# Kernel optimization log

Measured on AMD Instinct MI355X. Metric: run time of the kernel, lower is better.

## Reference

```python
import jax, jax.numpy as jnp
import numpy as np

N, E, NG = 10000, 160000, 64
HID, HEADS = 256, 4
NEG_SLOPE = 0.2


def setup_inputs() -> dict:
    key = jax.random.key(0)
    ks = jax.random.split(key, 20)
    s = 0.1
    inp = {
        "atom_features": jax.random.normal(ks[0], (N, 23), jnp.float32),
        "edge_index": jax.random.randint(ks[1], (2, E), 0, N),
        "batch": jnp.sort(jax.random.randint(ks[2], (N,), 0, NG)),
        "W1": jax.random.normal(ks[3], (23, HEADS * HID), jnp.float32) * s,
        "as1": jax.random.normal(ks[4], (HEADS, HID), jnp.float32) * s,
        "ad1": jax.random.normal(ks[5], (HEADS, HID), jnp.float32) * s,
        "b1": jnp.zeros((HEADS * HID,), jnp.float32),
        "W2": jax.random.normal(ks[6], (HEADS * HID, HEADS * HID), jnp.float32) * s,
        "as2": jax.random.normal(ks[7], (HEADS, HID), jnp.float32) * s,
        "ad2": jax.random.normal(ks[8], (HEADS, HID), jnp.float32) * s,
        "b2": jnp.zeros((HEADS * HID,), jnp.float32),
        "W3": jax.random.normal(ks[9], (HEADS * HID, HID), jnp.float32) * s,
        "as3": jax.random.normal(ks[10], (1, HID), jnp.float32) * s,
        "ad3": jax.random.normal(ks[11], (1, HID), jnp.float32) * s,
        "b3": jnp.zeros((HID,), jnp.float32),
        # MLP head
        "fc1_w": jax.random.normal(ks[12], (HID, HID // 2), jnp.float32) * s,
        "fc1_b": jnp.zeros((HID // 2,), jnp.float32),
        "fc2_w": jax.random.normal(ks[13], (HID // 2, 1), jnp.float32) * s,
        "fc2_b": jnp.zeros((1,), jnp.float32),
    }
    return inp


def gat_layer(x, W, att_src, att_dst, bias, src, dst, heads, ch):
    n = x.shape[0]
    h = (x @ W).reshape(n, heads, ch)                      # [N,H,C]
    a_s = jnp.sum(h * att_src, axis=-1)                    # [N,H]
    a_d = jnp.sum(h * att_dst, axis=-1)                    # [N,H]
    logits = jax.nn.leaky_relu(a_s[src] + a_d[dst], NEG_SLOPE)  # [E',H]
    m = jax.ops.segment_max(logits, dst, num_segments=n)
    m = jnp.where(jnp.isfinite(m), m, 0.0)
    e = jnp.exp(logits - m[dst])
    denom = jax.ops.segment_sum(e, dst, num_segments=n)
    alpha = e / (denom[dst] + 1e-16)                       # segment softmax over incoming edges
    out = jax.ops.segment_sum(alpha[:, :, None] * h[src], dst, num_segments=n)
    return out.reshape(n, heads * ch) + bias


def reference(atom_features, edge_index, batch,
              W1, as1, ad1, b1, W2, as2, ad2, b2, W3, as3, ad3, b3,
              fc1_w, fc1_b, fc2_w, fc2_b):
    n = atom_features.shape[0]
    loops = jnp.arange(n)
    src = jnp.concatenate([edge_index[0], loops])   # PyG GATConv adds self-loops
    dst = jnp.concatenate([edge_index[1], loops])

    x = jax.nn.elu(gat_layer(atom_features, W1, as1, ad1, b1, src, dst, HEADS, HID))
    x = jax.nn.elu(gat_layer(x, W2, as2, ad2, b2, src, dst, HEADS, HID))
    x = jax.nn.elu(gat_layer(x, W3, as3, ad3, b3, src, dst, 1, HID))
    # dropout: eval mode (training=False) -> identity

    # global mean pool over molecules
    sums = jax.ops.segment_sum(x, batch, num_segments=NG)
    counts = jax.ops.segment_sum(jnp.ones((n,), x.dtype), batch, num_segments=NG)
    features = sums / jnp.maximum(counts, 1.0)[:, None]    # [NG, HID]

    hmid = jax.nn.relu(features @ fc1_w + fc1_b)
    validity = hmid @ fc2_w + fc2_b                        # [NG, 1]
    return validity, features
```

## Files before the change

kernel.cpp:

```cpp
#include <hip/hip_runtime.h>
#include <hip/hip_bf16.h>
#include <math.h>

typedef unsigned short ushortT;
typedef __attribute__((ext_vector_type(8))) short short8;
typedef __attribute__((ext_vector_type(4))) float f32x4;

constexpr int NN   = 10000;
constexpr int MP   = 10112;
constexpr int EE   = 160000;
constexpr int ETOT = EE + NN;
constexpr int NG   = 64;
constexpr int HID  = 256;
constexpr int HEADS = 4;

__device__ __forceinline__ ushortT f2bf(float x) {
    __hip_bfloat16 h = __float2bfloat16(x);
    return *reinterpret_cast<ushortT*>(&h);
}
__device__ __forceinline__ float bf2f(ushortT x) {
    unsigned u = ((unsigned)x) << 16;
    return __uint_as_float(u);
}

__device__ __forceinline__ int xcd_swz(int flat, int nwg) {
    int q = nwg >> 3, r = nwg & 7;
    int xcd = flat & 7, j = flat >> 3;
    return (xcd < r ? xcd * (q + 1) : r * (q + 1) + (xcd - r) * q) + j;
}

__global__ __launch_bounds__(256) void setup_kernel(
        const float* __restrict__ W1, const float* __restrict__ as1,
        const float* __restrict__ ad1, float* __restrict__ wsv1,
        const float* __restrict__ W2, const float* __restrict__ as2,
        const float* __restrict__ ad2, float* __restrict__ wsv2,
        const float* __restrict__ W3, const float* __restrict__ as3,
        const float* __restrict__ ad3, float* __restrict__ wsv3,
        ushortT* __restrict__ wt2, ushortT* __restrict__ wt3,
        ushortT* __restrict__ b1p, const int* __restrict__ ei,
        int* __restrict__ cnt) {
    __shared__ float t[32][33];
    const int b = blockIdx.x, tid = threadIdx.x;
    if (b < 1280) {
        const float* W; ushortT* Wt; int N, n0, k0;
        if (b < 1024) { W = W2; Wt = wt2; N = 1024; n0 = (b & 31) * 32; k0 = (b >> 5) * 32; }
        else          { int b2 = b - 1024; W = W3; Wt = wt3; N = 256; n0 = (b2 & 7) * 32; k0 = (b2 >> 3) * 32; }
        const int K = 1024, Kp = 1024;
        int tx = tid & 31, ty = tid >> 5;
        for (int i = ty; i < 32; i += 8) {
            int k = k0 + i, n = n0 + tx;
            t[i][tx] = (k < K && n < N) ? W[(size_t)k * N + n] : 0.f;
        }
        __syncthreads();
        for (int i = ty; i < 32; i += 8) {
            int n = n0 + i, kp = k0 + tx;
            if (n < N && kp < Kp) Wt[(size_t)n * Kp + kp] = f2bf(t[tx][i]);
        }
    } else if (b < 1792) {
        int idx = (b - 1280) * 256 + tid;
        int n = idx >> 7, kp = idx & 127;
        int h = n >> 8, hk = kp >> 5, k = kp & 31;
        float v = (hk == h && k < 23) ? W1[(size_t)k * 1024 + n] : 0.f;
        b1p[idx] = f2bf(v);
    } else if (b < 4398) {
        int gw = (b - 1792) * 4 + (tid >> 6);
        int lane = tid & 63;
        const float *W, *atts, *attd; float* wsv; int heads, idx;
        if (gw < 184)            { W = W1; atts = as1; attd = ad1; wsv = wsv1; heads = 4; idx = gw; }
        else if (gw < 184 + 8192){ W = W2; atts = as2; attd = ad2; wsv = wsv2; heads = 4; idx = gw - 184; }
        else if (gw < 184 + 8192 + 2048) { W = W3; atts = as3; attd = ad3; wsv = wsv3; heads = 1; idx = gw - 184 - 8192; }
        else return;
        const int nout = 2 * heads;
        int k = idx / nout, o = idx - k * nout;
        int h = (o >= heads) ? (o - heads) : o;
        const float* att  = ((o >= heads) ? attd : atts) + h * HID;
        const float* wrow = W + (size_t)k * (heads * HID) + h * HID;
        float4 w4 = *(const float4*)(wrow + lane * 4);
        float4 a4 = *(const float4*)(att + lane * 4);
        float s = w4.x * a4.x + w4.y * a4.y + w4.z * a4.z + w4.w * a4.w;
        #pragma unroll
        for (int off = 1; off < 64; off <<= 1) s += __shfl_xor(s, off);
        if (lane == 0) wsv[(size_t)k * nout + o] = s;
    } else {
        int e = (b - 4398) * 256 + tid;
        if (e >= ETOT) return;
        int dst = (e < EE) ? ei[EE + e] : (e - EE);
        atomicAdd(&cnt[dst], 1);
    }
}

__global__ void scan_kernel(const int* __restrict__ cnt, int* __restrict__ row_ptr,
                            int* __restrict__ cursor) {
    __shared__ int part[256];
    int tid = threadIdx.x;
    const int chunk = (NN + 255) / 256;
    int s0 = tid * chunk;
    int s1 = min(NN, s0 + chunk);
    int sum = 0;
    for (int i = s0; i < s1; ++i) sum += cnt[i];
    part[tid] = sum;
    __syncthreads();
    for (int off = 1; off < 256; off <<= 1) {
        int v = (tid >= off) ? part[tid - off] : 0;
        __syncthreads();
        part[tid] += v;
        __syncthreads();
    }
    int run = (tid == 0) ? 0 : part[tid - 1];
    for (int i = s0; i < s1; ++i) {
        row_ptr[i] = run;
        cursor[i]  = run;
        run += cnt[i];
    }
    if (tid == 255) row_ptr[NN] = part[255];
}

__global__ void fill_dots1_kernel(const int* __restrict__ ei, int* __restrict__ cursor,
                                  int* __restrict__ col_src,
                                  const float* __restrict__ atom,
                                  const float* __restrict__ wsv1,
                                  float* __restrict__ a_s, float* __restrict__ a_d,
                                  int nfill) {
    int b = blockIdx.x;
    if (b < nfill) {
        int e = b * 256 + threadIdx.x;
        if (e >= ETOT) return;
        int src, dst;
        if (e < EE) { src = ei[e]; dst = ei[EE + e]; }
        else        { src = dst = e - EE; }
        int pos = atomicAdd(&cursor[dst], 1);
        col_src[pos] = src;
    } else {
        int n = (b - nfill) * 256 + threadIdx.x;
        if (n >= NN) return;
        float a[8] = {0.f, 0.f, 0.f, 0.f, 0.f, 0.f, 0.f, 0.f};
        #pragma unroll
        for (int k = 0; k < 23; ++k) {
            float x = atom[n * 23 + k];
            #pragma unroll
            for (int o = 0; o < 8; ++o) a[o] += x * wsv1[k * 8 + o];
        }
        #pragma unroll
        for (int h = 0; h < 4; ++h) { a_s[n * 4 + h] = a[h]; a_d[n * 4 + h] = a[4 + h]; }
    }
}

__global__ __launch_bounds__(256) void agg_atom_kernel(const float* __restrict__ atom,
                                                       const float* __restrict__ a_s,
                                                       const float* __restrict__ a_d,
                                                       const int* __restrict__ rowp,
                                                       const int* __restrict__ colv,
                                                       ushortT* __restrict__ Ap) {
    const int wv = threadIdx.x >> 6, lane = threadIdx.x & 63;
    const int i = blockIdx.x * 4 + wv;
    if (i >= NN) return;
    const int half = lane >> 5, c = lane & 31;
    const int start = rowp[i], end = rowp[i + 1];

    __shared__ float wsh[4][64][4];
    __shared__ int   ssh[4][64];

    float acc[4] = {0.f, 0.f, 0.f, 0.f};
    float den4[4] = {0.f, 0.f, 0.f, 0.f};
    for (int cb = start; cb < end; cb += 64) {
        int clen = min(64, end - cb);
        if (lane < clen) {
            int s = colv[cb + lane];
            ssh[wv][lane] = s;
            float4 as4 = *(const float4*)(a_s + (size_t)s * 4);
            float4 ad4 = *(const float4*)(a_d + (size_t)i * 4);
            float l0 = as4.x + ad4.x; l0 = (l0 >= 0.f) ? l0 : 0.2f * l0;
            float l1 = as4.y + ad4.y; l1 = (l1 >= 0.f) ? l1 : 0.2f * l1;
            float l2 = as4.z + ad4.z; l2 = (l2 >= 0.f) ? l2 : 0.2f * l2;
            float l3 = as4.w + ad4.w; l3 = (l3 >= 0.f) ? l3 : 0.2f * l3;
            float w0 = expf(l0), w1 = expf(l1), w2 = expf(l2), w3 = expf(l3);
            *reinterpret_cast<float4*>(&wsh[wv][lane][0]) = make_float4(w0, w1, w2, w3);
            den4[0] += w0; den4[1] += w1; den4[2] += w2; den4[3] += w3;
        }
        __builtin_amdgcn_wave_barrier();
        for (int e = half; e < clen; e += 2) {
            int s = ssh[wv][e];
            float x = (c < 23) ? atom[(size_t)s * 23 + c] : 0.f;
            acc[0] += wsh[wv][e][0] * x;
            acc[1] += wsh[wv][e][1] * x;
            acc[2] += wsh[wv][e][2] * x;
            acc[3] += wsh[wv][e][3] * x;
        }
        __builtin_amdgcn_wave_barrier();
    }
    #pragma unroll
    for (int h = 0; h < 4; ++h) acc[h] += __shfl_xor(acc[h], 32);
    #pragma unroll
    for (int off = 1; off < 64; off <<= 1) {
        den4[0] += __shfl_xor(den4[0], off);
        den4[1] += __shfl_xor(den4[1], off);
        den4[2] += __shfl_xor(den4[2], off);
        den4[3] += __shfl_xor(den4[3], off);
    }
    if (half == 0) {
        #pragma unroll
        for (int h = 0; h < 4; ++h) {
            float v = acc[h] / (den4[h] + 1e-16f);
            Ap[(size_t)i * 128 + h * 32 + c] = f2bf(v);
        }
    }
}

__device__ __forceinline__ void gload_lds16(const ushortT* gsrc, ushortT* ldst) {
    __builtin_amdgcn_global_load_lds(
        (const __attribute__((address_space(1))) unsigned int*)gsrc,
        (__attribute__((address_space(3))) unsigned int*)ldst, 16, 0, 0);
}

template<int MODE, int KS, int DOTS>
__global__ __launch_bounds__(512, 4) void gemm_bf16(const ushortT* __restrict__ A,
                                                    const ushortT* __restrict__ Bt,
                                                    ushortT* __restrict__ C,
                                                    const float* __restrict__ bias,
                                                    const float* __restrict__ wsv,
                                                    float* __restrict__ da_s,
                                                    float* __restrict__ da_d,
                                                    int N, int K, int nx, int ngemm) {
    __shared__ ushortT lds[2][2][128][KS];
    if ((int)blockIdx.x < ngemm) {
        const int tid  = threadIdx.x;
        const int lane = tid & 63, w = tid >> 6;
        const int wm = w >> 2, wn = w & 3;
        const int swz  = xcd_swz(blockIdx.x, ngemm);
        const int bx = swz % nx, by = swz / nx;
        const int row0 = by * 128;
        const int col0 = bx * 128;
        const int nt = K / KS;
        constexpr int GPR = KS / 8;
        constexpr int PT  = 128 * GPR / 512;

        auto stage = [&](int buf, int t) {
            int k0 = t * KS;
            #pragma unroll
            for (int i = 0; i < PT; ++i) {
                int g = i * 512 + tid;
                int row = g / GPR, gi = g % GPR;
                int sw = (KS == 64) ? (row & 7) : ((row & 3) ^ ((row >> 2) & 3));
                int koff = gi ^ sw;
                gload_lds16(A + (size_t)(row0 + row) * K + k0 + koff * 8,
                            &lds[buf][0][0][0] + g * 8);
                gload_lds16(Bt + (size_t)(col0 + row) * K + k0 + koff * 8,
                            &lds[buf][1][0][0] + g * 8);
            }
        };

        f32x4 acc[4][2] = {};
        const int lr = lane & 15, lk = lane >> 4;

        stage(0, 0);
        for (int t = 0; t < nt; ++t) {
            int buf = t & 1;
            __syncthreads();
            if (t + 1 < nt) stage(buf ^ 1, t + 1);
            const ushortT* baseA = &lds[buf][0][0][0];
            const ushortT* baseB = &lds[buf][1][0][0];
            #pragma unroll
            for (int kk = 0; kk < KS / 32; ++kk) {
                short8 a[4], b[2];
                #pragma unroll
                for (int m = 0; m < 4; ++m) {
                    int row = wm * 64 + m * 16 + lr;
                    int sw = (KS == 64) ? (row & 7) : ((row & 3) ^ ((row >> 2) & 3));
                    int gidx = (kk * 4 + lk) ^ sw;
                    a[m] = *(const short8*)(baseA + row * KS + gidx * 8);
                }
                #pragma unroll
                for (int n = 0; n < 2; ++n) {
                    int row = wn * 32 + n * 16 + lr;
                    int sw = (KS == 64) ? (row & 7) : ((row & 3) ^ ((row >> 2) & 3));
                    int gidx = (kk * 4 + lk) ^ sw;
                    b[n] = *(const short8*)(baseB + row * KS + gidx * 8);
                }
                #pragma unroll
                for (int m = 0; m < 4; ++m)
                    #pragma unroll
                    for (int n = 0; n < 2; ++n)
                        acc[m][n] = __builtin_amdgcn_mfma_f32_16x16x32_bf16(a[m], b[n], acc[m][n], 0, 0, 0);
            }
        }

        #pragma unroll
        for (int m = 0; m < 4; ++m) {
            #pragma unroll
            for (int n = 0; n < 2; ++n) {
                int col = col0 + wn * 32 + n * 16 + lr;
                float bv = (MODE == 1) ? bias[col] : 0.f;
                #pragma unroll
                for (int j = 0; j < 4; ++j) {
                    int rowg = row0 + wm * 64 + m * 16 + lk * 4 + j;
                    float v = acc[m][n][j];
                    if (MODE == 1) { v += bv; v = (v > 0.f) ? v : expm1f(v); }
                    C[(size_t)rowg * N + col] = f2bf(v);
                }
            }
        }
    } else if (DOTS == 2) {
        int gw = ((int)blockIdx.x - ngemm) * 8 + (threadIdx.x >> 6);
        int lane = threadIdx.x & 63;
        if (gw >= NN) return;
        const ushortT* row = A + (size_t)gw * 1024 + lane * 16;
        short8 v0 = *(const short8*)row;
        short8 v1 = *(const short8*)(row + 8);
        float ps[8] = {0.f, 0.f, 0.f, 0.f, 0.f, 0.f, 0.f, 0.f};
        const float* wb = wsv + (size_t)lane * 16 * 8;
        #pragma unroll
        for (int c = 0; c < 8; ++c) {
            float xv = bf2f((ushortT)v0[c]);
            #pragma unroll
            for (int o = 0; o < 8; ++o) ps[o] += xv * wb[c * 8 + o];
        }
        #pragma unroll
        for (int c = 0; c < 8; ++c) {
            float xv = bf2f((ushortT)v1[c]);
            #pragma unroll
            for (int o = 0; o < 8; ++o) ps[o] += xv * wb[(8 + c) * 8 + o];
        }
        #pragma unroll
        for (int off = 1; off < 64; off <<= 1) {
            #pragma unroll
            for (int o = 0; o < 8; ++o) ps[o] += __shfl_xor(ps[o], off);
        }
        if (lane == 0) {
            #pragma unroll
            for (int h = 0; h < 4; ++h) { da_s[gw * 4 + h] = ps[h]; da_d[gw * 4 + h] = ps[4 + h]; }
        }
    } else if (DOTS == 3) {
        int gw = ((int)blockIdx.x - ngemm) * 8 + (threadIdx.x >> 6);
        int lane = threadIdx.x & 63;
        if (gw >= NN) return;
        const ushortT* row = A + (size_t)gw * 1024 + lane * 16;
        short8 v0 = *(const short8*)row;
        short8 v1 = *(const short8*)(row + 8);
        float p0 = 0.f, p1 = 0.f;
        const int c0 = lane * 16;
        #pragma unroll
        for (int c = 0; c < 8; ++c) {
            float xv = bf2f((ushortT)v0[c]);
            float2 w2 = *(const float2*)(wsv + (size_t)(c0 + c) * 2);
            p0 += xv * w2.x; p1 += xv * w2.y;
        }
        #pragma unroll
        for (int c = 0; c < 8; ++c) {
            float xv = bf2f((ushortT)v1[c]);
            float2 w2 = *(const float2*)(wsv + (size_t)(c0 + 8 + c) * 2);
            p0 += xv * w2.x; p1 += xv * w2.y;
        }
        #pragma unroll
        for (int off = 1; off < 64; off <<= 1) {
            p0 += __shfl_xor(p0, off);
            p1 += __shfl_xor(p1, off);
        }
        if (lane == 0) { da_s[gw] = p0; da_d[gw] = p1; }
    }
}

__global__ __launch_bounds__(256) void gat_agg_h4(const ushortT* __restrict__ hfeat,
                                                  const float* __restrict__ a_s,
                                                  const float* __restrict__ a_d,
                                                  const int* __restrict__ rowp,
                                                  const int* __restrict__ colv,
                                                  const float* __restrict__ bias,
                                                  ushortT* __restrict__ out16) {
    const int wv = threadIdx.x >> 6, lane = threadIdx.x & 63;
    const int i = blockIdx.x * 4 + wv;
    if (i >= NN) return;
    const int c0 = lane * 16;
    const int hh = c0 >> 8;
    const int start = rowp[i], end = rowp[i + 1];

    __shared__ float wsh[4][64][4];
    __shared__ int   ssh[4][64];

    float acc[16];
    #pragma unroll
    for (int c = 0; c < 16; ++c) acc[c] = 0.f;
    float den4[4] = {0.f, 0.f, 0.f, 0.f};

    for (int cb = start; cb < end; cb += 64) {
        int clen = min(64, end - cb);
        if (lane < clen) {
            int s = colv[cb + lane];
            ssh[wv][lane] = s;
            float4 as4 = *(const float4*)(a_s + (size_t)s * 4);
            float4 ad4 = *(const float4*)(a_d + (size_t)i * 4);
            float l0 = as4.x + ad4.x; l0 = (l0 >= 0.f) ? l0 : 0.2f * l0;
            float l1 = as4.y + ad4.y; l1 = (l1 >= 0.f) ? l1 : 0.2f * l1;
            float l2 = as4.z + ad4.z; l2 = (l2 >= 0.f) ? l2 : 0.2f * l2;
            float l3 = as4.w + ad4.w; l3 = (l3 >= 0.f) ? l3 : 0.2f * l3;
            float w0 = expf(l0), w1 = expf(l1), w2 = expf(l2), w3 = expf(l3);
            *reinterpret_cast<float4*>(&wsh[wv][lane][0]) = make_float4(w0, w1, w2, w3);
            den4[0] += w0; den4[1] += w1; den4[2] += w2; den4[3] += w3;
        }
        __builtin_amdgcn_wave_barrier();
        int e = 0;
        for (; e + 4 <= clen; e += 4) {
            int sa = ssh[wv][e], sb = ssh[wv][e + 1], sc = ssh[wv][e + 2], sd = ssh[wv][e + 3];
            const ushortT* pa = hfeat + (size_t)sa * 1024 + c0;
            const ushortT* pb = hfeat + (size_t)sb * 1024 + c0;
            const ushortT* pc = hfeat + (size_t)sc * 1024 + c0;
            const ushortT* pd = hfeat + (size_t)sd * 1024 + c0;
            short8 va0 = *(const short8*)pa,       va1 = *(const short8*)(pa + 8);
            short8 vb0 = *(const short8*)pb,       vb1 = *(const short8*)(pb + 8);
            short8 vc0 = *(const short8*)pc,       vc1 = *(const short8*)(pc + 8);
            short8 vd0 = *(const short8*)pd,       vd1 = *(const short8*)(pd + 8);
            float wa = wsh[wv][e][hh],     wb = wsh[wv][e + 1][hh];
            float wc = wsh[wv][e + 2][hh], wd = wsh[wv][e + 3][hh];
            #pragma unroll
            for (int j = 0; j < 8; ++j) {
                acc[j]     += wa * bf2f((ushortT)va0[j]) + wb * bf2f((ushortT)vb0[j])
                            + wc * bf2f((ushortT)vc0[j]) + wd * bf2f((ushortT)vd0[j]);
                acc[8 + j] += wa * bf2f((ushortT)va1[j]) + wb * bf2f((ushortT)vb1[j])
                            + wc * bf2f((ushortT)vc1[j]) + wd * bf2f((ushortT)vd1[j]);
            }
        }
        for (; e < clen; ++e) {
            int s = ssh[wv][e];
            float wgt = wsh[wv][e][hh];
            const ushortT* p = hfeat + (size_t)s * 1024 + c0;
            short8 v0 = *(const short8*)p;
            short8 v1 = *(const short8*)(p + 8);
            #pragma unroll
            for (int j = 0; j < 8; ++j) {
                acc[j]     += wgt * bf2f((ushortT)v0[j]);
                acc[8 + j] += wgt * bf2f((ushortT)v1[j]);
            }
        }
        __builtin_amdgcn_wave_barrier();
    }

    #pragma unroll
    for (int off = 1; off < 64; off <<= 1) {
        den4[0] += __shfl_xor(den4[0], off);
        den4[1] += __shfl_xor(den4[1], off);
        den4[2] += __shfl_xor(den4[2], off);
        den4[3] += __shfl_xor(den4[3], off);
    }
    float den = (hh == 0) ? den4[0] : (hh == 1) ? den4[1] : (hh == 2) ? den4[2] : den4[3];
    float inv = 1.f / (den + 1e-16f);

    ushortT pk[16];
    #pragma unroll
    for (int c = 0; c < 16; ++c) {
        float v = acc[c] * inv + bias[c0 + c];
        v = (v > 0.f) ? v : expm1f(v);
        pk[c] = f2bf(v);
    }
    *reinterpret_cast<short8*>(out16 + (size_t)i * 1024 + c0)     = *reinterpret_cast<short8*>(&pk[0]);
    *reinterpret_cast<short8*>(out16 + (size_t)i * 1024 + c0 + 8) = *reinterpret_cast<short8*>(&pk[8]);
}

__global__ __launch_bounds__(256) void gat_agg_h1(const ushortT* __restrict__ hfeat,
                                                  const float* __restrict__ a_s,
                                                  const float* __restrict__ a_d,
                                                  const int* __restrict__ rowp,
                                                  const int* __restrict__ colv,
                                                  const float* __restrict__ bias,
                                                  float* __restrict__ outf) {
    const int wv = threadIdx.x >> 6, lane = threadIdx.x & 63;
    const int i = blockIdx.x * 4 + wv;
    if (i >= NN) return;
    const int c0 = lane * 4;
    const int start = rowp[i], end = rowp[i + 1];
    const float adi = a_d[i];

    __shared__ float wsh[4][64];
    __shared__ int   ssh[4][64];

    float acc[4] = {0.f, 0.f, 0.f, 0.f};
    float den = 0.f;

    for (int cb = start; cb < end; cb += 64) {
        int clen = min(64, end - cb);
        if (lane < clen) {
            int s = colv[cb + lane];
            ssh[wv][lane] = s;
            float l = a_s[s] + adi;
            l = (l >= 0.f) ? l : 0.2f * l;
            float w0 = expf(l);
            wsh[wv][lane] = w0;
            den += w0;
        }
        __builtin_amdgcn_wave_barrier();
        int e = 0;
        for (; e + 4 <= clen; e += 4) {
            int sa = ssh[wv][e], sb = ssh[wv][e + 1], sc = ssh[wv][e + 2], sd = ssh[wv][e + 3];
            ushort4 va = *(const ushort4*)(hfeat + (size_t)sa * 256 + c0);
            ushort4 vb = *(const ushort4*)(hfeat + (size_t)sb * 256 + c0);
            ushort4 vc = *(const ushort4*)(hfeat + (size_t)sc * 256 + c0);
            ushort4 vd = *(const ushort4*)(hfeat + (size_t)sd * 256 + c0);
            float wa = wsh[wv][e], wb2 = wsh[wv][e + 1], wc2 = wsh[wv][e + 2], wd2 = wsh[wv][e + 3];
            acc[0] += wa * bf2f(va.x) + wb2 * bf2f(vb.x) + wc2 * bf2f(vc.x) + wd2 * bf2f(vd.x);
            acc[1] += wa * bf2f(va.y) + wb2 * bf2f(vb.y) + wc2 * bf2f(vc.y) + wd2 * bf2f(vd.y);
            acc[2] += wa * bf2f(va.z) + wb2 * bf2f(vb.z) + wc2 * bf2f(vc.z) + wd2 * bf2f(vd.z);
            acc[3] += wa * bf2f(va.w) + wb2 * bf2f(vb.w) + wc2 * bf2f(vc.w) + wd2 * bf2f(vd.w);
        }
        for (; e < clen; ++e) {
            int s = ssh[wv][e];
            float wgt = wsh[wv][e];
            ushort4 v = *(const ushort4*)(hfeat + (size_t)s * 256 + c0);
            acc[0] += wgt * bf2f(v.x); acc[1] += wgt * bf2f(v.y);
            acc[2] += wgt * bf2f(v.z); acc[3] += wgt * bf2f(v.w);
        }
        __builtin_amdgcn_wave_barrier();
    }

    #pragma unroll
    for (int off = 1; off < 64; off <<= 1) den += __shfl_xor(den, off);
    float inv = 1.f / (den + 1e-16f);

    float4 o4;
    float v0 = acc[0] * inv + bias[c0 + 0]; o4.x = (v0 > 0.f) ? v0 : expm1f(v0);
    float v1 = acc[1] * inv + bias[c0 + 1]; o4.y = (v1 > 0.f) ? v1 : expm1f(v1);
    float v2 = acc[2] * inv + bias[c0 + 2]; o4.z = (v2 > 0.f) ? v2 : expm1f(v2);
    float v3 = acc[3] * inv + bias[c0 + 3]; o4.w = (v3 > 0.f) ? v3 : expm1f(v3);
    *reinterpret_cast<float4*>(outf + (size_t)i * 256 + c0) = o4;
}

__global__ void pool_mlp(const float* __restrict__ x,
                         const int* __restrict__ batch,
                         const float* __restrict__ fc1_w,
                         const float* __restrict__ fc1_b,
                         const float* __restrict__ fc2_w,
                         const float* __restrict__ fc2_b,
                         float* __restrict__ out) {
    int g = blockIdx.x, tid = threadIdx.x;
    int lo = 0, hi = NN;
    while (lo < hi) { int mid = (lo + hi) >> 1; if (batch[mid] < g) lo = mid + 1; else hi = mid; }
    int s0 = lo;
    lo = 0; hi = NN;
    while (lo < hi) { int mid = (lo + hi) >> 1; if (batch[mid] < g + 1) lo = mid + 1; else hi = mid; }
    int s1 = lo;

    float acc = 0.f;
    for (int n = s0; n < s1; ++n) acc += x[(size_t)n * HID + tid];
    float cnt = (float)(s1 - s0);
    float feat = acc / fmaxf(cnt, 1.f);
    out[NG + g * HID + tid] = feat;

    __shared__ float fsh[HID];
    fsh[tid] = feat;
    __syncthreads();
    __shared__ float r2[128];
    if (tid < 128) {
        float a = fc1_b[tid];
        for (int c = 0; c < HID; ++c) a += fsh[c] * fc1_w[c * 128 + tid];
        a = fmaxf(a, 0.f);
        r2[tid] = a * fc2_w[tid];
    }
    __syncthreads();
    for (int s2 = 64; s2 > 0; s2 >>= 1) {
        if (tid < s2) r2[tid] += r2[tid + s2];
        __syncthreads();
    }
    if (tid == 0) out[g] = r2[0] + fc2_b[0];
}

extern "C" void kernel_launch(void* const* d_in, const int* in_sizes, int n_in,
                              void* d_out, int out_size, void* d_ws, size_t ws_size,
                              hipStream_t stream) {
    const float* atom  = (const float*)d_in[0];
    const int*   ei    = (const int*)  d_in[1];
    const int*   batch = (const int*)  d_in[2];
    const float* W1  = (const float*)d_in[3];
    const float* as1 = (const float*)d_in[4];
    const float* ad1 = (const float*)d_in[5];
    const float* b1  = (const float*)d_in[6];
    const float* W2  = (const float*)d_in[7];
    const float* as2 = (const float*)d_in[8];
    const float* ad2 = (const float*)d_in[9];
    const float* b2  = (const float*)d_in[10];
    const float* W3  = (const float*)d_in[11];
    const float* as3 = (const float*)d_in[12];
    const float* ad3 = (const float*)d_in[13];
    const float* b3  = (const float*)d_in[14];
    const float* fc1w = (const float*)d_in[15];
    const float* fc1b = (const float*)d_in[16];
    const float* fc2w = (const float*)d_in[17];
    const float* fc2b = (const float*)d_in[18];
    float* out = (float*)d_out;

    ushortT* h16  = (ushortT*)d_ws;
    ushortT* x16  = h16 + (size_t)MP * 1024;
    ushortT* Ap   = x16 + (size_t)MP * 1024;
    ushortT* b1p  = Ap + (size_t)MP * 128;
    ushortT* wt2  = b1p + 1024 * 128;
    ushortT* wt3  = wt2 + 1024 * 1024;
    float*   x3   = (float*)(wt3 + 256 * 1024);
    float*   asL1 = x3 + (size_t)NN * 256;
    float*   adL1 = asL1 + (size_t)NN * 4;
    float*   asL2 = adL1 + (size_t)NN * 4;
    float*   adL2 = asL2 + (size_t)NN * 4;
    float*   asL3 = adL2 + (size_t)NN * 4;
    float*   adL3 = asL3 + NN;
    float*   wsv1 = adL3 + NN;
    float*   wsv2 = wsv1 + 23 * 8;
    float*   wsv3 = wsv2 + 1024 * 8;
    int*   cnt    = (int*)(wsv3 + 1024 * 2);
    int*   rowp   = cnt + NN;
    int*   cursor = rowp + NN + 1;
    int*   col    = cursor + NN;

    dim3 blk(256), blk512(512);
    const int gagg  = (NN + 3) / 4;
    const int gy    = MP / 128;
    const int nd8   = (NN + 7) / 8;

    hipMemsetAsync(cnt, 0, NN * sizeof(int), stream);
    const int ecnt_blocks = (ETOT + 255) / 256;
    setup_kernel<<<4398 + ecnt_blocks, blk, 0, stream>>>(
        W1, as1, ad1, wsv1, W2, as2, ad2, wsv2,
        W3, as3, ad3, wsv3, wt2, wt3, b1p, ei, cnt);

    scan_kernel<<<1, blk, 0, stream>>>(cnt, rowp, cursor);
    fill_dots1_kernel<<<ecnt_blocks + (NN + 255) / 256, blk, 0, stream>>>(
        ei, cursor, col, atom, wsv1, asL1, adL1, ecnt_blocks);

    agg_atom_kernel<<<gagg, blk, 0, stream>>>(atom, asL1, adL1, rowp, col, Ap);
    gemm_bf16<1, 32, 0><<<8 * gy, blk512, 0, stream>>>(Ap, b1p, x16, b1, nullptr, nullptr, nullptr,
                                                       1024, 128, 8, 8 * gy);

    gemm_bf16<0, 64, 2><<<8 * gy + nd8, blk512, 0, stream>>>(x16, wt2, h16, nullptr, wsv2,
                                                             asL2, adL2, 1024, 1024, 8, 8 * gy);
    gat_agg_h4<<<gagg, blk, 0, stream>>>(h16, asL2, adL2, rowp, col, b2, x16);

    gemm_bf16<0, 64, 3><<<2 * gy + nd8, blk512, 0, stream>>>(x16, wt3, h16, nullptr, wsv3,
                                                             asL3, adL3, 256, 1024, 2, 2 * gy);
    gat_agg_h1<<<gagg, blk, 0, stream>>>(h16, asL3, adL3, rowp, col, b3, x3);

    pool_mlp<<<NG, blk, 0, stream>>>(x3, batch, fc1w, fc1b, fc2w, fc2b, out);
}
```

Baseline: 290.7 us.

## Triple-buffer GEMM LDS pipeline with KS=32 and unroll gather by 8

Replaces the double-buffered GEMM K-loop with a triple-buffered pipeline at a fixed K-step of 32. It waits on vmcnt counters and issues one barrier per step, so two stages of global-to-LDS loads stay in flight. Launch bounds rise to 6 waves per SIMD to push occupancy. Separately, the single-head aggregation gathers 8 neighbour rows per iteration instead of 4, giving more memory-level parallelism. Risks include register pressure from the new launch bounds, more loop iterations for the K=1024 GEMMs, and the correctness of the manual vmcnt waits.

New measurement: 293.4 us. Within noise of the previous version (+0.9%).

```diff
diff --git a/kernel.cpp b/kernel.cpp
--- a/kernel.cpp
+++ b/kernel.cpp
@@ -212,8 +212,8 @@
         (__attribute__((address_space(3))) unsigned int*)ldst, 16, 0, 0);
 }
 
-template<int MODE, int KS, int DOTS>
-__global__ __launch_bounds__(512, 4) void gemm_bf16(const ushortT* __restrict__ A,
+template<int MODE, int DOTS>
+__global__ __launch_bounds__(512, 6) void gemm_bf16(const ushortT* __restrict__ A,
                                                     const ushortT* __restrict__ Bt,
                                                     ushortT* __restrict__ C,
                                                     const float* __restrict__ bias,
@@ -221,7 +221,8 @@
                                                     float* __restrict__ da_s,
                                                     float* __restrict__ da_d,
                                                     int N, int K, int nx, int ngemm) {
-    __shared__ ushortT lds[2][2][128][KS];
+    constexpr int KS = 32;
+    __shared__ ushortT lds[3][2][128][KS];
     if ((int)blockIdx.x < ngemm) {
         const int tid  = threadIdx.x;
         const int lane = tid & 63, w = tid >> 6;
@@ -231,57 +232,52 @@
         const int row0 = by * 128;
         const int col0 = bx * 128;
         const int nt = K / KS;
-        constexpr int GPR = KS / 8;
-        constexpr int PT  = 128 * GPR / 512;
 
         auto stage = [&](int buf, int t) {
             int k0 = t * KS;
-            #pragma unroll
-            for (int i = 0; i < PT; ++i) {
-                int g = i * 512 + tid;
-                int row = g / GPR, gi = g % GPR;
-                int sw = (KS == 64) ? (row & 7) : ((row & 3) ^ ((row >> 2) & 3));
-                int koff = gi ^ sw;
-                gload_lds16(A + (size_t)(row0 + row) * K + k0 + koff * 8,
-                            &lds[buf][0][0][0] + g * 8);
-                gload_lds16(Bt + (size_t)(col0 + row) * K + k0 + koff * 8,
-                            &lds[buf][1][0][0] + g * 8);
-            }
+            int g = tid;
+            int row = g >> 2, gi = g & 3;
+            int sw = (row & 3) ^ ((row >> 2) & 3);
+            int koff = gi ^ sw;
+            gload_lds16(A + (size_t)(row0 + row) * K + k0 + koff * 8,
+                        &lds[buf][0][0][0] + g * 8);
+            gload_lds16(Bt + (size_t)(col0 + row) * K + k0 + koff * 8,
+                        &lds[buf][1][0][0] + g * 8);
         };
 
         f32x4 acc[4][2] = {};
         const int lr = lane & 15, lk = lane >> 4;
 
         stage(0, 0);
+        stage(1, 1);
+        int buf = 0;
         for (int t = 0; t < nt; ++t) {
-            int buf = t & 1;
-            __syncthreads();
-            if (t + 1 < nt) stage(buf ^ 1, t + 1);
+            if (t + 1 < nt) asm volatile("s_waitcnt vmcnt(2)" ::: "memory");
+            else            asm volatile("s_waitcnt vmcnt(0)" ::: "memory");
+            __builtin_amdgcn_s_barrier();
+            asm volatile("" ::: "memory");
+            if (t + 2 < nt) stage((buf + 2 >= 3) ? buf - 1 : buf + 2, t + 2);
             const ushortT* baseA = &lds[buf][0][0][0];
             const ushortT* baseB = &lds[buf][1][0][0];
-            #pragma unroll
-            for (int kk = 0; kk < KS / 32; ++kk) {
-                short8 a[4], b[2];
+            short8 a[4], b[2];
+            #pragma unroll
+            for (int m = 0; m < 4; ++m) {
+                int row = wm * 64 + m * 16 + lr;
+                int sw = (row & 3) ^ ((row >> 2) & 3);
+                a[m] = *(const short8*)(baseA + row * KS + ((lk ^ sw) * 8));
+            }
+            #pragma unroll
+            for (int n = 0; n < 2; ++n) {
+                int row = wn * 32 + n * 16 + lr;
+                int sw = (row & 3) ^ ((row >> 2) & 3);
+                b[n] = *(const short8*)(baseB + row * KS + ((lk ^ sw) * 8));
+            }
+            #pragma unroll
+            for (int m = 0; m < 4; ++m)
                 #pragma unroll
-                for (int m = 0; m < 4; ++m) {
-                    int row = wm * 64 + m * 16 + lr;
-                    int sw = (KS == 64) ? (row & 7) : ((row & 3) ^ ((row >> 2) & 3));
-                    int gidx = (kk * 4 + lk) ^ sw;
-                    a[m] = *(const short8*)(baseA + row * KS + gidx * 8);
-                }
-                #pragma unroll
-                for (int n = 0; n < 2; ++n) {
-                    int row = wn * 32 + n * 16 + lr;
-                    int sw = (KS == 64) ? (row & 7) : ((row & 3) ^ ((row >> 2) & 3));
-                    int gidx = (kk * 4 + lk) ^ sw;
-                    b[n] = *(const short8*)(baseB + row * KS + gidx * 8);
-                }
-                #pragma unroll
-                for (int m = 0; m < 4; ++m)
-                    #pragma unroll
-                    for (int n = 0; n < 2; ++n)
-                        acc[m][n] = __builtin_amdgcn_mfma_f32_16x16x32_bf16(a[m], b[n], acc[m][n], 0, 0, 0);
-            }
+                for (int n = 0; n < 2; ++n)
+                    acc[m][n] = __builtin_amdgcn_mfma_f32_16x16x32_bf16(a[m], b[n], acc[m][n], 0, 0, 0);
+            buf = (buf + 1 >= 3) ? 0 : buf + 1;
         }
 
         #pragma unroll
@@ -487,17 +483,22 @@
         }
         __builtin_amdgcn_wave_barrier();
         int e = 0;
-        for (; e + 4 <= clen; e += 4) {
-            int sa = ssh[wv][e], sb = ssh[wv][e + 1], sc = ssh[wv][e + 2], sd = ssh[wv][e + 3];
-            ushort4 va = *(const ushort4*)(hfeat + (size_t)sa * 256 + c0);
-            ushort4 vb = *(const ushort4*)(hfeat + (size_t)sb * 256 + c0);
-            ushort4 vc = *(const ushort4*)(hfeat + (size_t)sc * 256 + c0);
-            ushort4 vd = *(const ushort4*)(hfeat + (size_t)sd * 256 + c0);
-            float wa = wsh[wv][e], wb2 = wsh[wv][e + 1], wc2 = wsh[wv][e + 2], wd2 = wsh[wv][e + 3];
-            acc[0] += wa * bf2f(va.x) + wb2 * bf2f(vb.x) + wc2 * bf2f(vc.x) + wd2 * bf2f(vd.x);
-            acc[1] += wa * bf2f(va.y) + wb2 * bf2f(vb.y) + wc2 * bf2f(vc.y) + wd2 * bf2f(vd.y);
-            acc[2] += wa * bf2f(va.z) + wb2 * bf2f(vb.z) + wc2 * bf2f(vc.z) + wd2 * bf2f(vd.z);
-            acc[3] += wa * bf2f(va.w) + wb2 * bf2f(vb.w) + wc2 * bf2f(vc.w) + wd2 * bf2f(vd.w);
+        for (; e + 8 <= clen; e += 8) {
+            ushort4 v[8];
+            float wv8[8];
+            #pragma unroll
+            for (int j = 0; j < 8; ++j) {
+                int s = ssh[wv][e + j];
+                v[j] = *(const ushort4*)(hfeat + (size_t)s * 256 + c0);
+                wv8[j] = wsh[wv][e + j];
+            }
+            #pragma unroll
+            for (int j = 0; j < 8; ++j) {
+                acc[0] += wv8[j] * bf2f(v[j].x);
+                acc[1] += wv8[j] * bf2f(v[j].y);
+                acc[2] += wv8[j] * bf2f(v[j].z);
+                acc[3] += wv8[j] * bf2f(v[j].w);
+            }
         }
         for (; e < clen; ++e) {
             int s = ssh[wv][e];
@@ -621,15 +622,15 @@
         ei, cursor, col, atom, wsv1, asL1, adL1, ecnt_blocks);
 
     agg_atom_kernel<<<gagg, blk, 0, stream>>>(atom, asL1, adL1, rowp, col, Ap);
-    gemm_bf16<1, 32, 0><<<8 * gy, blk512, 0, stream>>>(Ap, b1p, x16, b1, nullptr, nullptr, nullptr,
-                                                       1024, 128, 8, 8 * gy);
-
-    gemm_bf16<0, 64, 2><<<8 * gy + nd8, blk512, 0, stream>>>(x16, wt2, h16, nullptr, wsv2,
-                                                             asL2, adL2, 1024, 1024, 8, 8 * gy);
+    gemm_bf16<1, 0><<<8 * gy, blk512, 0, stream>>>(Ap, b1p, x16, b1, nullptr, nullptr, nullptr,
+                                                   1024, 128, 8, 8 * gy);
+
+    gemm_bf16<0, 2><<<8 * gy + nd8, blk512, 0, stream>>>(x16, wt2, h16, nullptr, wsv2,
+                                                         asL2, adL2, 1024, 1024, 8, 8 * gy);
     gat_agg_h4<<<gagg, blk, 0, stream>>>(h16, asL2, adL2, rowp, col, b2, x16);
 
-    gemm_bf16<0, 64, 3><<<2 * gy + nd8, blk512, 0, stream>>>(x16, wt3, h16, nullptr, wsv3,
-                                                             asL3, adL3, 256, 1024, 2, 2 * gy);
+    gemm_bf16<0, 3><<<2 * gy + nd8, blk512, 0, stream>>>(x16, wt3, h16, nullptr, wsv3,
+                                                         asL3, adL3, 256, 1024, 2, 2 * gy);
     gat_agg_h1<<<gagg, blk, 0, stream>>>(h16, asL3, adL3, rowp, col, b3, x3);
 
     pool_mlp<<<NG, blk, 0, stream>>>(x3, batch, fc1w, fc1b, fc2w, fc2b, out);
```
